# Optimization experiments

Hardware: AMD Instinct MI355X
Metric: run time of the kernel (lower is better)

## Reference

```python
import jax, jax.numpy as jnp
import numpy as np

B, S, HID = 2, 2048, 4096
H, KV, D = 32, 8, 128      # num_heads, num_kv_heads, head_dim
G = H // KV                 # num_key_value_groups
N = 16                      # num_neighbors
RH = HID // 4               # r_hidden_size (compression_factor=4)


def setup_inputs() -> dict:
    key = jax.random.key(0)
    ks = jax.random.split(key, 6)
    return {
        "hidden_states": jax.random.normal(ks[0], (B, S, HID), jnp.float32),
        "retrieved_hidden_states": jax.random.normal(ks[1], (B, S, N, RH), jnp.float32),
        # nn.Linear weights [out_features, in_features], std = in_features**-0.5
        "Wq": jax.random.normal(ks[2], (H * D, HID), jnp.float32) * HID ** -0.5,
        "Wk": jax.random.normal(ks[3], (KV * D, RH), jnp.float32) * RH ** -0.5,
        "Wv": jax.random.normal(ks[4], (KV * D, RH), jnp.float32) * RH ** -0.5,
        "Wo": jax.random.normal(ks[5], (HID, H * D), jnp.float32) * (H * D) ** -0.5,
    }


def reference(hidden_states, retrieved_hidden_states, Wq, Wk, Wv, Wo):
    b, s, hid = hidden_states.shape
    n = retrieved_hidden_states.shape[2]
    scaler = D ** -0.5
    # queries: [b,s,H*D] -> grouped [b,s,KV,G,D] (head h = kv_head*G + g, matching repeat_kv)
    q = (hidden_states @ Wq.T * scaler).reshape(b, s, KV, G, D)
    # keys/values: torch computes [b,s,n,KV*D] then flat-views as [b,s,KV,n,D]; replicate exactly
    k = (retrieved_hidden_states @ Wk.T).reshape(b, s, KV, n, D)
    v = (retrieved_hidden_states @ Wv.T).reshape(b, s, KV, n, D)
    # per-query attention over n neighbors; grouped einsum avoids materializing repeat_kv expand
    scores = jnp.einsum('bskgd,bsknd->bskgn', q, k)   # [b,s,KV,G,n]
    attn = jax.nn.softmax(scores, axis=-1)
    out = jnp.einsum('bskgn,bsknd->bskgd', attn, v).reshape(b, s, H * D)
    return out @ Wo.T
```

## Files before the change

kernel.cpp:

```cpp
#include <hip/hip_runtime.h>
#include <hip/hip_bf16.h>
#include <stdint.h>

#define DEV_INLINE __device__ __forceinline__

typedef __attribute__((ext_vector_type(4))) float f32x4;
typedef __attribute__((ext_vector_type(8))) __bf16 bf16x8;
typedef __attribute__((ext_vector_type(8))) unsigned short u16x8;

constexpr int Hh = 32, KVc = 8, Dd = 128, Gg = 4, Nn = 16;

DEV_INLINE unsigned short f32_to_bf16(float f) {
  unsigned u = __float_as_uint(f);
  u += 0x7fffu + ((u >> 16) & 1u);
  return (unsigned short)(u >> 16);
}
DEV_INLINE float bf16_lo(unsigned u) { return __uint_as_float(u << 16); }
DEV_INLINE float bf16_hi(unsigned u) { return __uint_as_float(u & 0xffff0000u); }

__global__ void cast_f32_bf16_kernel(const float* __restrict__ src,
                                     unsigned short* __restrict__ dst,
                                     int n4, float scale) {
  int i = blockIdx.x * blockDim.x + threadIdx.x;
  int stride = gridDim.x * blockDim.x;
  const f32x4* s4 = reinterpret_cast<const f32x4*>(src);
  ushort4* d4 = reinterpret_cast<ushort4*>(dst);
  for (; i < n4; i += stride) {
    f32x4 v = s4[i];
    ushort4 o;
    o.x = f32_to_bf16(v.x * scale);
    o.y = f32_to_bf16(v.y * scale);
    o.z = f32_to_bf16(v.z * scale);
    o.w = f32_to_bf16(v.w * scale);
    d4[i] = o;
  }
}

template <bool OUT_BF16>
__global__ __launch_bounds__(512) void gemm256_kernel(
    const unsigned short* __restrict__ A,
    const unsigned short* __restrict__ Bw,
    void* __restrict__ Cout,
    int M, int N, int K) {
  __shared__ alignas(16) unsigned short Als[4][256 * 32];
  __shared__ alignas(16) unsigned short Bls[4][256 * 32];
  const int tid = threadIdx.x;
  const int wave = tid >> 6, lane = tid & 63;
  const int wm = wave >> 2, wn = wave & 3;
  const int lrow = lane & 15, lhi = lane >> 4;
  const int swslot = (lhi ^ ((lrow >> 1) & 3)) << 4;

  const int ntn = N >> 8;
  const int nwg = gridDim.x, bid = blockIdx.x;
  const int swz = ((nwg & 7) == 0) ? ((bid & 7) * (nwg >> 3) + (bid >> 3)) : bid;
  const int tm = swz / ntn, tn = swz - tm * ntn;

  const unsigned short* Abase = A + (long)tm * 256 * K;
  const unsigned short* Bbase = Bw + (long)tn * 256 * K;
  const int ktiles = K >> 5;

  auto stage = [&](const unsigned short* gbase, unsigned short* lslot, int k0) {
#pragma unroll
    for (int j = 0; j < 2; ++j) {
      int c = (j << 9) + tid;
      int row = c >> 2;
      int gslot = (c & 3) ^ ((row >> 1) & 3);
      const unsigned short* g = gbase + (long)row * K + k0 + (gslot << 3);
      int ldsoff = (((j << 9) + (wave << 6)) << 4);
      __builtin_amdgcn_global_load_lds(
          (const __attribute__((address_space(1))) unsigned int*)g,
          (__attribute__((address_space(3))) unsigned int*)((char*)lslot + ldsoff),
          16, 0, 0);
    }
  };

  f32x4 acc[8][4];
#pragma unroll
  for (int m = 0; m < 8; ++m)
#pragma unroll
    for (int n = 0; n < 4; ++n) acc[m][n] = {0.f, 0.f, 0.f, 0.f};

#pragma unroll
  for (int p = 0; p < 3; ++p) {
    if (p < ktiles) {
      stage(Abase, Als[p], p << 5);
      stage(Bbase, Bls[p], p << 5);
    }
  }
  if (ktiles > 2) asm volatile("s_waitcnt vmcnt(8)" ::: "memory");
  else            asm volatile("s_waitcnt vmcnt(0)" ::: "memory");
  __builtin_amdgcn_s_barrier();

  bf16x8 afr[4], bfr[4];
  for (int t = 0; t < ktiles; ++t) {
    const int slot = t & 3, ps = (t + 3) & 3;
    const char* Ac = (const char*)Als[slot];
    const char* Bc = (const char*)Bls[slot];

#pragma unroll
    for (int n = 0; n < 4; ++n)
      bfr[n] = *reinterpret_cast<const bf16x8*>(
          Bc + (((wn << 6) + (n << 4) + lrow) << 6) + swslot);
#pragma unroll
    for (int m = 0; m < 4; ++m)
      afr[m] = *reinterpret_cast<const bf16x8*>(
          Ac + (((wm << 7) + (m << 4) + lrow) << 6) + swslot);
    if (t + 3 < ktiles) stage(Abase, Als[ps], (t + 3) << 5);
    __builtin_amdgcn_s_barrier();
    asm volatile("s_waitcnt lgkmcnt(0)");
    __builtin_amdgcn_s_setprio(1);
#pragma unroll
    for (int m = 0; m < 4; ++m)
#pragma unroll
      for (int n = 0; n < 4; ++n)
        acc[m][n] = __builtin_amdgcn_mfma_f32_16x16x32_bf16(afr[m], bfr[n],
                                                            acc[m][n], 0, 0, 0);
    __builtin_amdgcn_s_setprio(0);
    __builtin_amdgcn_s_barrier();

#pragma unroll
    for (int m = 0; m < 4; ++m)
      afr[m] = *reinterpret_cast<const bf16x8*>(
          Ac + (((wm << 7) + 64 + (m << 4) + lrow) << 6) + swslot);
    if (t + 3 < ktiles) stage(Bbase, Bls[ps], (t + 3) << 5);
    __builtin_amdgcn_s_barrier();
    asm volatile("s_waitcnt lgkmcnt(0)");
    __builtin_amdgcn_s_setprio(1);
#pragma unroll
    for (int m = 0; m < 4; ++m)
#pragma unroll
      for (int n = 0; n < 4; ++n)
        acc[m + 4][n] = __builtin_amdgcn_mfma_f32_16x16x32_bf16(
            afr[m], bfr[n], acc[m + 4][n], 0, 0, 0);
    __builtin_amdgcn_s_setprio(0);
    if (t + 3 < ktiles)      asm volatile("s_waitcnt vmcnt(8)" ::: "memory");
    else if (t + 2 < ktiles) asm volatile("s_waitcnt vmcnt(4)" ::: "memory");
    else if (t + 1 < ktiles) asm volatile("s_waitcnt vmcnt(0)" ::: "memory");
    __builtin_amdgcn_s_barrier();
  }

#pragma unroll
  for (int m = 0; m < 8; ++m) {
#pragma unroll
    for (int n = 0; n < 4; ++n) {
      long r0 = (long)tm * 256 + (wm << 7) + (m << 4) + (lhi << 2);
      long c0 = (long)tn * 256 + (wn << 6) + (n << 4) + lrow;
#pragma unroll
      for (int r = 0; r < 4; ++r) {
        float v = acc[m][n][r];
        if constexpr (OUT_BF16)
          ((unsigned short*)Cout)[(r0 + r) * N + c0] = f32_to_bf16(v);
        else
          ((float*)Cout)[(r0 + r) * N + c0] = v;
      }
    }
  }
}

__global__ __launch_bounds__(256) void attn_kernel(
    const unsigned short* __restrict__ Q,
    const unsigned short* __restrict__ Kf,
    const unsigned short* __restrict__ Vf,
    unsigned short* __restrict__ O) {
  const int tid = threadIdx.x;
  const int wave = tid >> 6;
  const int lane = tid & 63;
  const int sl = blockIdx.x * 4 + wave;
  const int bs = sl >> 3;
  const int kv = sl & 7;
  const int g = lane >> 4;
  const int i = lane & 15;

  const unsigned short* qrow = Q + (long)bs * (Hh * Dd) + (kv * Gg + g) * Dd;
  const int ni = 2 * kv + (i >> 3);
  const unsigned short* krow =
      Kf + ((long)bs * Nn + ni) * (KVc * Dd) + (i & 7) * Dd;

  float s = 0.f;
#pragma unroll
  for (int c = 0; c < 16; ++c) {
    uint4 qu = *reinterpret_cast<const uint4*>(qrow + c * 8);
    uint4 ku = *reinterpret_cast<const uint4*>(krow + c * 8);
    s += bf16_lo(qu.x) * bf16_lo(ku.x) + bf16_hi(qu.x) * bf16_hi(ku.x);
    s += bf16_lo(qu.y) * bf16_lo(ku.y) + bf16_hi(qu.y) * bf16_hi(ku.y);
    s += bf16_lo(qu.z) * bf16_lo(ku.z) + bf16_hi(qu.z) * bf16_hi(ku.z);
    s += bf16_lo(qu.w) * bf16_lo(ku.w) + bf16_hi(qu.w) * bf16_hi(ku.w);
  }

  float mx = s;
#pragma unroll
  for (int off = 8; off >= 1; off >>= 1) mx = fmaxf(mx, __shfl_xor(mx, off));
  float p = __expf(s - mx);
  float sum = p;
#pragma unroll
  for (int off = 8; off >= 1; off >>= 1) sum += __shfl_xor(sum, off);
  p = p / sum;

  float o[8] = {0.f, 0.f, 0.f, 0.f, 0.f, 0.f, 0.f, 0.f};
  const long vbase = (long)bs * Nn * (KVc * Dd);
#pragma unroll
  for (int ii = 0; ii < 16; ++ii) {
    float pi = __shfl(p, (lane & 48) | ii);
    const unsigned short* vrow = Vf + vbase +
        (long)(2 * kv + (ii >> 3)) * (KVc * Dd) + (ii & 7) * Dd + i * 8;
    uint4 vu = *reinterpret_cast<const uint4*>(vrow);
    o[0] += pi * bf16_lo(vu.x); o[1] += pi * bf16_hi(vu.x);
    o[2] += pi * bf16_lo(vu.y); o[3] += pi * bf16_hi(vu.y);
    o[4] += pi * bf16_lo(vu.z); o[5] += pi * bf16_hi(vu.z);
    o[6] += pi * bf16_lo(vu.w); o[7] += pi * bf16_hi(vu.w);
  }
  u16x8 ov;
#pragma unroll
  for (int d = 0; d < 8; ++d) ov[d] = f32_to_bf16(o[d]);
  *reinterpret_cast<u16x8*>(O + (long)bs * (Hh * Dd) + (kv * Gg + g) * Dd +
                            i * 8) = ov;
}

extern "C" void kernel_launch(void* const* d_in, const int* in_sizes, int n_in,
                              void* d_out, int out_size, void* d_ws,
                              size_t ws_size, hipStream_t stream) {
  (void)in_sizes; (void)n_in; (void)out_size; (void)ws_size;
  const float* hs = (const float*)d_in[0];
  const float* rhs = (const float*)d_in[1];
  const float* Wq = (const float*)d_in[2];
  const float* Wk = (const float*)d_in[3];
  const float* Wv = (const float*)d_in[4];
  const float* Wo = (const float*)d_in[5];
  float* out = (float*)d_out;

  char* ws = (char*)d_ws;
  size_t off = 0;
  auto alloc = [&](size_t bytes) { char* p = ws + off; off += bytes; return p; };
  unsigned short* hsb  = (unsigned short*)alloc(16777216ull * 2);
  unsigned short* Wqb  = (unsigned short*)alloc(16777216ull * 2);
  unsigned short* rhsb = (unsigned short*)alloc(67108864ull * 2);
  unsigned short* Wkb  = (unsigned short*)alloc(1048576ull * 2);
  unsigned short* Wvb  = (unsigned short*)alloc(1048576ull * 2);
  unsigned short* Wob  = (unsigned short*)alloc(16777216ull * 2);
  unsigned short* Qb   = (unsigned short*)alloc(16777216ull * 2);
  unsigned short* Kb   = (unsigned short*)alloc(67108864ull * 2);
  unsigned short* Vb   = (unsigned short*)alloc(67108864ull * 2);
  unsigned short* Ab   = (unsigned short*)alloc(16777216ull * 2);

  const float scaler = 0.08838834764831845f;

  cast_f32_bf16_kernel<<<2048, 256, 0, stream>>>(hs, hsb, 16777216 / 4, 1.f);
  cast_f32_bf16_kernel<<<2048, 256, 0, stream>>>(Wq, Wqb, 16777216 / 4, scaler);
  cast_f32_bf16_kernel<<<4096, 256, 0, stream>>>(rhs, rhsb, 67108864 / 4, 1.f);
  cast_f32_bf16_kernel<<<512, 256, 0, stream>>>(Wk, Wkb, 1048576 / 4, 1.f);
  cast_f32_bf16_kernel<<<512, 256, 0, stream>>>(Wv, Wvb, 1048576 / 4, 1.f);
  cast_f32_bf16_kernel<<<2048, 256, 0, stream>>>(Wo, Wob, 16777216 / 4, 1.f);

  gemm256_kernel<true><<<256, 512, 0, stream>>>(hsb, Wqb, Qb, 4096, 4096, 4096);
  gemm256_kernel<true><<<1024, 512, 0, stream>>>(rhsb, Wkb, Kb, 65536, 1024, 1024);
  gemm256_kernel<true><<<1024, 512, 0, stream>>>(rhsb, Wvb, Vb, 65536, 1024, 1024);
  attn_kernel<<<8192, 256, 0, stream>>>(Qb, Kb, Vb, Ab);
  gemm256_kernel<false><<<256, 512, 0, stream>>>(Ab, Wob, out, 4096, 4096, 4096);
}
```

Measured before the change: 864.4 us.

## Replace 256x256 GEMM tiles with 128x128 tiles and three-stage single-barrier pipeline

Switches all four GEMMs from a 512-thread 256x256 tile kernel to a 256-thread 128x128 tile kernel. It uses a 3-slot LDS ring, a prefetch distance of two, and one barrier per k-step. The goal is more blocks per CU for latency hiding and less synchronisation per k-step. The trade-off is lower arithmetic intensity per tile, with more global and LDS traffic per FLOP.

```diff
diff --git a/kernel.cpp b/kernel.cpp
--- a/kernel.cpp
+++ b/kernel.cpp
@@ -37,77 +37,81 @@
 }
 
 template <bool OUT_BF16>
-__global__ __launch_bounds__(512) void gemm256_kernel(
+__global__ __launch_bounds__(256, 3) void gemm128_kernel(
     const unsigned short* __restrict__ A,
     const unsigned short* __restrict__ Bw,
     void* __restrict__ Cout,
     int M, int N, int K) {
-  __shared__ alignas(16) unsigned short Als[4][256 * 32];
-  __shared__ alignas(16) unsigned short Bls[4][256 * 32];
+  __shared__ alignas(16) unsigned short Als[3][4096];
+  __shared__ alignas(16) unsigned short Bls[3][4096];
   const int tid = threadIdx.x;
   const int wave = tid >> 6, lane = tid & 63;
-  const int wm = wave >> 2, wn = wave & 3;
+  const int wr = wave >> 1, wc = wave & 1;
   const int lrow = lane & 15, lhi = lane >> 4;
   const int swslot = (lhi ^ ((lrow >> 1) & 3)) << 4;
 
-  const int ntn = N >> 8;
+  const int ntn = N >> 7;
   const int nwg = gridDim.x, bid = blockIdx.x;
-  const int swz = ((nwg & 7) == 0) ? ((bid & 7) * (nwg >> 3) + (bid >> 3)) : bid;
+  const int swz = (bid & 7) * (nwg >> 3) + (bid >> 3);
   const int tm = swz / ntn, tn = swz - tm * ntn;
 
-  const unsigned short* Abase = A + (long)tm * 256 * K;
-  const unsigned short* Bbase = Bw + (long)tn * 256 * K;
+  const unsigned short* Abase = A + (long)tm * 128 * K;
+  const unsigned short* Bbase = Bw + (long)tn * 128 * K;
   const int ktiles = K >> 5;
 
   auto stage = [&](const unsigned short* gbase, unsigned short* lslot, int k0) {
 #pragma unroll
     for (int j = 0; j < 2; ++j) {
-      int c = (j << 9) + tid;
+      int c = (j << 8) + tid;
       int row = c >> 2;
-      int gslot = (c & 3) ^ ((row >> 1) & 3);
-      const unsigned short* g = gbase + (long)row * K + k0 + (gslot << 3);
-      int ldsoff = (((j << 9) + (wave << 6)) << 4);
+      int lg = (c & 3) ^ ((row >> 1) & 3);
+      const unsigned short* g = gbase + (long)row * K + k0 + (lg << 3);
+      int ldsoff = ((j << 8) + (wave << 6)) << 4;
       __builtin_amdgcn_global_load_lds(
           (const __attribute__((address_space(1))) unsigned int*)g,
-          (__attribute__((address_space(3))) unsigned int*)((char*)lslot + ldsoff),
+          (__attribute__((address_space(3))) unsigned int*)((char*)lslot +
+                                                            ldsoff),
           16, 0, 0);
     }
   };
 
-  f32x4 acc[8][4];
-#pragma unroll
-  for (int m = 0; m < 8; ++m)
+  f32x4 acc[4][4];
+#pragma unroll
+  for (int m = 0; m < 4; ++m)
 #pragma unroll
     for (int n = 0; n < 4; ++n) acc[m][n] = {0.f, 0.f, 0.f, 0.f};
 
-#pragma unroll
-  for (int p = 0; p < 3; ++p) {
-    if (p < ktiles) {
-      stage(Abase, Als[p], p << 5);
-      stage(Bbase, Bls[p], p << 5);
-    }
-  }
-  if (ktiles > 2) asm volatile("s_waitcnt vmcnt(8)" ::: "memory");
-  else            asm volatile("s_waitcnt vmcnt(0)" ::: "memory");
+  stage(Abase, Als[0], 0);
+  stage(Bbase, Bls[0], 0);
+  if (ktiles > 1) {
+    stage(Abase, Als[1], 32);
+    stage(Bbase, Bls[1], 32);
+    asm volatile("s_waitcnt vmcnt(4)" ::: "memory");
+  } else {
+    asm volatile("s_waitcnt vmcnt(0)" ::: "memory");
+  }
   __builtin_amdgcn_s_barrier();
 
-  bf16x8 afr[4], bfr[4];
+  int slot = 0;
   for (int t = 0; t < ktiles; ++t) {
-    const int slot = t & 3, ps = (t + 3) & 3;
     const char* Ac = (const char*)Als[slot];
     const char* Bc = (const char*)Bls[slot];
-
+    bf16x8 afr[4], bfr[4];
+#pragma unroll
+    for (int m = 0; m < 4; ++m)
+      afr[m] = *reinterpret_cast<const bf16x8*>(
+          Ac + (((wr << 6) + (m << 4) + lrow) << 6) + swslot);
 #pragma unroll
     for (int n = 0; n < 4; ++n)
       bfr[n] = *reinterpret_cast<const bf16x8*>(
-          Bc + (((wn << 6) + (n << 4) + lrow) << 6) + swslot);
-#pragma unroll
-    for (int m = 0; m < 4; ++m)
-      afr[m] = *reinterpret_cast<const bf16x8*>(
-          Ac + (((wm << 7) + (m << 4) + lrow) << 6) + swslot);
-    if (t + 3 < ktiles) stage(Abase, Als[ps], (t + 3) << 5);
-    __builtin_amdgcn_s_barrier();
-    asm volatile("s_waitcnt lgkmcnt(0)");
+          Bc + (((wc << 6) + (n << 4) + lrow) << 6) + swslot);
+
+    if (t + 2 < ktiles) {
+      int ps = slot + 2; if (ps >= 3) ps -= 3;
+      stage(Abase, Als[ps], (t + 2) << 5);
+      stage(Bbase, Bls[ps], (t + 2) << 5);
+    }
+
     __builtin_amdgcn_s_setprio(1);
 #pragma unroll
     for (int m = 0; m < 4; ++m)
@@ -116,35 +120,20 @@
         acc[m][n] = __builtin_amdgcn_mfma_f32_16x16x32_bf16(afr[m], bfr[n],
                                                             acc[m][n], 0, 0, 0);
     __builtin_amdgcn_s_setprio(0);
-    __builtin_amdgcn_s_barrier();
-
-#pragma unroll
-    for (int m = 0; m < 4; ++m)
-      afr[m] = *reinterpret_cast<const bf16x8*>(
-          Ac + (((wm << 7) + 64 + (m << 4) + lrow) << 6) + swslot);
-    if (t + 3 < ktiles) stage(Bbase, Bls[ps], (t + 3) << 5);
-    __builtin_amdgcn_s_barrier();
-    asm volatile("s_waitcnt lgkmcnt(0)");
-    __builtin_amdgcn_s_setprio(1);
-#pragma unroll
-    for (int m = 0; m < 4; ++m)
-#pragma unroll
-      for (int n = 0; n < 4; ++n)
-        acc[m + 4][n] = __builtin_amdgcn_mfma_f32_16x16x32_bf16(
-            afr[m], bfr[n], acc[m + 4][n], 0, 0, 0);
-    __builtin_amdgcn_s_setprio(0);
-    if (t + 3 < ktiles)      asm volatile("s_waitcnt vmcnt(8)" ::: "memory");
-    else if (t + 2 < ktiles) asm volatile("s_waitcnt vmcnt(4)" ::: "memory");
+
+    if (t + 2 < ktiles)      asm volatile("s_waitcnt vmcnt(4)" ::: "memory");
     else if (t + 1 < ktiles) asm volatile("s_waitcnt vmcnt(0)" ::: "memory");
     __builtin_amdgcn_s_barrier();
-  }
-
-#pragma unroll
-  for (int m = 0; m < 8; ++m) {
+    ++slot; if (slot >= 3) slot = 0;
+  }
+
+  const int rbase = lhi << 2;
+#pragma unroll
+  for (int m = 0; m < 4; ++m) {
 #pragma unroll
     for (int n = 0; n < 4; ++n) {
-      long r0 = (long)tm * 256 + (wm << 7) + (m << 4) + (lhi << 2);
-      long c0 = (long)tn * 256 + (wn << 6) + (n << 4) + lrow;
+      long r0 = (long)tm * 128 + (wr << 6) + (m << 4) + rbase;
+      long c0 = (long)tn * 128 + (wc << 6) + (n << 4) + lrow;
 #pragma unroll
       for (int r = 0; r < 4; ++r) {
         float v = acc[m][n][r];
@@ -251,9 +240,9 @@
   cast_f32_bf16_kernel<<<512, 256, 0, stream>>>(Wv, Wvb, 1048576 / 4, 1.f);
   cast_f32_bf16_kernel<<<2048, 256, 0, stream>>>(Wo, Wob, 16777216 / 4, 1.f);
 
-  gemm256_kernel<true><<<256, 512, 0, stream>>>(hsb, Wqb, Qb, 4096, 4096, 4096);
-  gemm256_kernel<true><<<1024, 512, 0, stream>>>(rhsb, Wkb, Kb, 65536, 1024, 1024);
-  gemm256_kernel<true><<<1024, 512, 0, stream>>>(rhsb, Wvb, Vb, 65536, 1024, 1024);
+  gemm128_kernel<true><<<1024, 256, 0, stream>>>(hsb, Wqb, Qb, 4096, 4096, 4096);
+  gemm128_kernel<true><<<4096, 256, 0, stream>>>(rhsb, Wkb, Kb, 65536, 1024, 1024);
+  gemm128_kernel<true><<<4096, 256, 0, stream>>>(rhsb, Wvb, Vb, 65536, 1024, 1024);
   attn_kernel<<<8192, 256, 0, stream>>>(Qb, Kb, Vb, Ab);
-  gemm256_kernel<false><<<256, 512, 0, stream>>>(Ab, Wob, out, 4096, 4096, 4096);
-}
+  gemm128_kernel<false><<<1024, 256, 0, stream>>>(Ab, Wob, out, 4096, 4096, 4096);
+}
```

Result: slower. 966.9 us (+11.9%).
